# Optimization experiments

Hardware: AMD Instinct MI355X
Metric: run time of the kernel (lower is better)

Reference implementation:

```python
import jax, jax.numpy as jnp
import numpy as np

B, HK, HV, DK, DV, K = 256, 16, 32, 128, 128, 4
QKV = DK * HK * 2 + DV * HV  # 8192
EPS = 1e-6


def setup_inputs() -> dict:
    key = jax.random.key(0)
    ks = jax.random.split(key, 8)
    return dict(
        mixed_qkv=jax.random.normal(ks[0], (B, QKV), jnp.float32),
        a=jax.random.normal(ks[1], (B, HV), jnp.float32),
        b=jax.random.normal(ks[2], (B, HV), jnp.float32),
        conv_state=jax.random.normal(ks[3], (B, QKV, K - 1), jnp.float32),
        conv_weights=jax.random.normal(ks[4], (QKV, K), jnp.float32) * 0.1,
        dt_bias=jax.random.normal(ks[5], (HV,), jnp.float32),
        alog=jax.random.normal(ks[6], (HV,), jnp.float32) * 0.1,
        ssm_state=jax.random.normal(ks[7], (B, HV, DK, DV), jnp.float32) * 0.05,
    )


def reference(mixed_qkv, a, b, conv_state, conv_weights, dt_bias, alog, ssm_state):
    # --- causal_conv1d_update (decode step, seq=1): window = [cached K-1 steps, new token]
    x_cat = jnp.concatenate([conv_state, mixed_qkv[:, :, None]], axis=-1)  # [B, QKV, K]
    conv_out = jax.nn.silu(jnp.einsum('bck,ck->bc', x_cat, conv_weights))  # [B, QKV]

    # --- split q/k/v heads
    qkv = conv_out.reshape(B, 2 * HK + HV, DK)
    q, k, v = qkv[:, :HK], qkv[:, HK:2 * HK], qkv[:, 2 * HK:]  # [B,HK,DK]x2, [B,HV,DV]

    # --- fused_gdn_gating: g = -exp(A_log) * softplus(a + dt_bias); beta = sigmoid(b)
    g = -jnp.exp(alog)[None, :] * jax.nn.softplus(a + dt_bias[None, :])  # [B, HV]
    beta = jax.nn.sigmoid(b)  # [B, HV]

    # --- GQA expand k heads -> v heads
    rep = HV // HK
    q = jnp.repeat(q, rep, axis=1)  # [B, HV, DK]
    k = jnp.repeat(k, rep, axis=1)

    # --- qk l2-norm (in-kernel) + default scale d_k^-0.5 on q
    q = q / jnp.sqrt(jnp.sum(q * q, axis=-1, keepdims=True) + EPS)
    k = k / jnp.sqrt(jnp.sum(k * k, axis=-1, keepdims=True) + EPS)
    q = q * (DK ** -0.5)

    # --- single-step gated delta rule recurrence
    S = ssm_state * jnp.exp(g)[:, :, None, None]          # decay: [B,HV,DK,DV]
    kv_mem = jnp.einsum('bhkv,bhk->bhv', S, k)            # k^T S
    dv = (v - kv_mem) * beta[:, :, None]                  # delta correction
    S = S + k[:, :, :, None] * dv[:, :, None, :]          # rank-1 update
    o = jnp.einsum('bhkv,bhk->bhv', S, q)                 # [B, HV, DV]
    return o
```

## Files before the change

kernel.cpp:

```cpp
#include <hip/hip_runtime.h>
#include <math.h>

#define NB   256
#define NHK  16
#define NHV  32
#define NDK  128
#define NDV  128
#define NQKV 8192

__global__ __launch_bounds__(256) void gdn_decode_kernel(
    const float* __restrict__ mixed_qkv,
    const float* __restrict__ a_in,
    const float* __restrict__ b_in,
    const float* __restrict__ conv_state,
    const float* __restrict__ conv_w,
    const float* __restrict__ dt_bias,
    const float* __restrict__ alog,
    const float* __restrict__ ssm_state,
    float* __restrict__ out)
{
    const int bh  = blockIdx.x;
    const int b   = bh >> 5;
    const int h   = bh & 31;
    const int tid = threadIdx.x;

    __shared__ float qL[NDK], kL[NDK], vL[NDV];
    __shared__ float redq[128], redk[128], redqk[128];
    __shared__ __align__(16) float p1[8][NDV];
    __shared__ __align__(16) float p2[8][NDV];
    __shared__ float sc[2];

    for (int i = tid; i < 384; i += 256) {
        int seg  = i >> 7;
        int lane = i & 127;
        int head = (seg == 0) ? (h >> 1) : (seg == 1 ? 16 + (h >> 1) : 32 + h);
        int c    = head * 128 + lane;
        const float* cs = conv_state + ((size_t)b * NQKV + c) * 3;
        const float* w  = conv_w + (size_t)c * 4;
        float x   = mixed_qkv[(size_t)b * NQKV + c];
        float pre = cs[0]*w[0] + cs[1]*w[1] + cs[2]*w[2] + x*w[3];
        float y   = pre / (1.0f + expf(-pre));
        if (seg == 0)      qL[lane] = y;
        else if (seg == 1) kL[lane] = y;
        else               vL[lane] = y;
    }
    if (tid == 0) {
        float av = a_in[bh] + dt_bias[h];
        float sp = fmaxf(av, 0.0f) + log1pf(expf(-fabsf(av)));
        float g  = -expf(alog[h]) * sp;
        sc[0] = expf(g);
        sc[1] = 1.0f / (1.0f + expf(-b_in[bh]));
    }
    __syncthreads();

    if (tid < 128) {
        float qv   = qL[tid];
        redq[tid]  = qv * qv;
        redqk[tid] = qv * kL[tid];
    } else {
        float kv        = kL[tid - 128];
        redk[tid - 128] = kv * kv;
    }
    __syncthreads();
    for (int s = 64; s > 0; s >>= 1) {
        if (tid < s) { redq[tid] += redq[tid + s]; redqk[tid] += redqk[tid + s]; }
        else if (tid >= 128 && tid < 128 + s) { redk[tid-128] += redk[tid-128+s]; }
        __syncthreads();
    }
    const float invq = (1.0f / sqrtf(redq[0] + 1e-6f)) * 0.08838834764831845f;
    const float invk =  1.0f / sqrtf(redk[0] + 1e-6f);
    const float kq   = redqk[0] * invq * invk;
    if (tid < 128) qL[tid] *= invq;
    else           kL[tid - 128] *= invk;
    __syncthreads();

    const int vg = tid & 31;
    const int ks = tid >> 5;
    const float4* Srow = (const float4*)(ssm_state + (size_t)bh * NDK * NDV);
    float4 a1 = make_float4(0.f,0.f,0.f,0.f);
    float4 a2 = make_float4(0.f,0.f,0.f,0.f);
    #pragma unroll
    for (int kk = 0; kk < 16; ++kk) {
        int k = ks * 16 + kk;
        float4 s = Srow[k * 32 + vg];
        float kw = kL[k], qw = qL[k];
        a1.x = fmaf(s.x, kw, a1.x); a1.y = fmaf(s.y, kw, a1.y);
        a1.z = fmaf(s.z, kw, a1.z); a1.w = fmaf(s.w, kw, a1.w);
        a2.x = fmaf(s.x, qw, a2.x); a2.y = fmaf(s.y, qw, a2.y);
        a2.z = fmaf(s.z, qw, a2.z); a2.w = fmaf(s.w, qw, a2.w);
    }
    *(float4*)&p1[ks][vg * 4] = a1;
    *(float4*)&p2[ks][vg * 4] = a2;
    __syncthreads();

    if (tid < 128) {
        float t1 = 0.f, t2 = 0.f;
        #pragma unroll
        for (int s = 0; s < 8; ++s) { t1 += p1[s][tid]; t2 += p2[s][tid]; }
        const float eg   = sc[0];
        const float beta = sc[1];
        float dv = (vL[tid] - eg * t1) * beta;
        out[(size_t)bh * NDV + tid] = fmaf(eg, t2, kq * dv);
    }
}

extern "C" void kernel_launch(void* const* d_in, const int* in_sizes, int n_in,
                              void* d_out, int out_size, void* d_ws, size_t ws_size,
                              hipStream_t stream) {
    const float* mixed = (const float*)d_in[0];
    const float* a     = (const float*)d_in[1];
    const float* bg    = (const float*)d_in[2];
    const float* cs    = (const float*)d_in[3];
    const float* cw    = (const float*)d_in[4];
    const float* dtb   = (const float*)d_in[5];
    const float* al    = (const float*)d_in[6];
    const float* ssm   = (const float*)d_in[7];
    float* out = (float*)d_out;

    gdn_decode_kernel<<<NB * NHV, 256, 0, stream>>>(mixed, a, bg, cs, cw, dtb, al, ssm, out);
}
```

Baseline: 103.5 us.

## Process both GQA value heads per block sharing q/k conv and norm

```diff
diff --git a/kernel.cpp b/kernel.cpp
--- a/kernel.cpp
+++ b/kernel.cpp
@@ -7,6 +7,8 @@
 #define NDK  128
 #define NDV  128
 #define NQKV 8192
+
+typedef float f32x4 __attribute__((ext_vector_type(4)));
 
 __global__ __launch_bounds__(256) void gdn_decode_kernel(
     const float* __restrict__ mixed_qkv,
@@ -19,21 +21,25 @@
     const float* __restrict__ ssm_state,
     float* __restrict__ out)
 {
-    const int bh  = blockIdx.x;
-    const int b   = bh >> 5;
-    const int h   = bh & 31;
+    const int bid = blockIdx.x;
+    const int b   = bid >> 4;
+    const int hk  = bid & 15;
     const int tid = threadIdx.x;
+    const int h0  = 2 * hk;
+    const size_t bh0 = (size_t)b * NHV + h0;
 
-    __shared__ float qL[NDK], kL[NDK], vL[NDV];
+    __shared__ float qL[NDK], kL[NDK], vL[2][NDV];
     __shared__ float redq[128], redk[128], redqk[128];
     __shared__ __align__(16) float p1[8][NDV];
     __shared__ __align__(16) float p2[8][NDV];
-    __shared__ float sc[2];
+    __shared__ float sc_eg[2], sc_beta[2];
 
-    for (int i = tid; i < 384; i += 256) {
+    #pragma unroll
+    for (int ii = 0; ii < 2; ++ii) {
+        int i    = tid + ii * 256;
         int seg  = i >> 7;
         int lane = i & 127;
-        int head = (seg == 0) ? (h >> 1) : (seg == 1 ? 16 + (h >> 1) : 32 + h);
+        int head = (seg == 0) ? hk : (seg == 1) ? (16 + hk) : (32 + h0 + (seg - 2));
         int c    = head * 128 + lane;
         const float* cs = conv_state + ((size_t)b * NQKV + c) * 3;
         const float* w  = conv_w + (size_t)c * 4;
@@ -42,14 +48,16 @@
         float y   = pre / (1.0f + expf(-pre));
         if (seg == 0)      qL[lane] = y;
         else if (seg == 1) kL[lane] = y;
-        else               vL[lane] = y;
+        else               vL[seg - 2][lane] = y;
     }
-    if (tid == 0) {
+    if (tid < 2) {
+        size_t bh = bh0 + tid;
+        int    h  = h0 + tid;
         float av = a_in[bh] + dt_bias[h];
         float sp = fmaxf(av, 0.0f) + log1pf(expf(-fabsf(av)));
         float g  = -expf(alog[h]) * sp;
-        sc[0] = expf(g);
-        sc[1] = 1.0f / (1.0f + expf(-b_in[bh]));
+        sc_eg[tid]   = expf(g);
+        sc_beta[tid] = 1.0f / (1.0f + expf(-b_in[bh]));
     }
     __syncthreads();
 
@@ -76,31 +84,46 @@
 
     const int vg = tid & 31;
     const int ks = tid >> 5;
-    const float4* Srow = (const float4*)(ssm_state + (size_t)bh * NDK * NDV);
-    float4 a1 = make_float4(0.f,0.f,0.f,0.f);
-    float4 a2 = make_float4(0.f,0.f,0.f,0.f);
+    const f32x4* S0 = (const f32x4*)(ssm_state + bh0 * (NDK * NDV));
+    const f32x4* S1 = S0 + (NDK * NDV / 4);
+    f32x4 a1_0 = {0.f,0.f,0.f,0.f}, a2_0 = {0.f,0.f,0.f,0.f};
+    f32x4 a1_1 = {0.f,0.f,0.f,0.f}, a2_1 = {0.f,0.f,0.f,0.f};
     #pragma unroll
     for (int kk = 0; kk < 16; ++kk) {
         int k = ks * 16 + kk;
-        float4 s = Srow[k * 32 + vg];
+        f32x4 s0 = __builtin_nontemporal_load(&S0[k * 32 + vg]);
+        f32x4 s1 = __builtin_nontemporal_load(&S1[k * 32 + vg]);
         float kw = kL[k], qw = qL[k];
-        a1.x = fmaf(s.x, kw, a1.x); a1.y = fmaf(s.y, kw, a1.y);
-        a1.z = fmaf(s.z, kw, a1.z); a1.w = fmaf(s.w, kw, a1.w);
-        a2.x = fmaf(s.x, qw, a2.x); a2.y = fmaf(s.y, qw, a2.y);
-        a2.z = fmaf(s.z, qw, a2.z); a2.w = fmaf(s.w, qw, a2.w);
+        a1_0 += s0 * kw;
+        a2_0 += s0 * qw;
+        a1_1 += s1 * kw;
+        a2_1 += s1 * qw;
     }
-    *(float4*)&p1[ks][vg * 4] = a1;
-    *(float4*)&p2[ks][vg * 4] = a2;
+
+    *(f32x4*)&p1[ks][vg * 4] = a1_0;
+    *(f32x4*)&p2[ks][vg * 4] = a2_0;
     __syncthreads();
-
     if (tid < 128) {
         float t1 = 0.f, t2 = 0.f;
         #pragma unroll
         for (int s = 0; s < 8; ++s) { t1 += p1[s][tid]; t2 += p2[s][tid]; }
-        const float eg   = sc[0];
-        const float beta = sc[1];
-        float dv = (vL[tid] - eg * t1) * beta;
-        out[(size_t)bh * NDV + tid] = fmaf(eg, t2, kq * dv);
+        const float eg   = sc_eg[0];
+        const float beta = sc_beta[0];
+        float dv = (vL[0][tid] - eg * t1) * beta;
+        out[bh0 * NDV + tid] = fmaf(eg, t2, kq * dv);
+    }
+    __syncthreads();
+    *(f32x4*)&p1[ks][vg * 4] = a1_1;
+    *(f32x4*)&p2[ks][vg * 4] = a2_1;
+    __syncthreads();
+    if (tid < 128) {
+        float t1 = 0.f, t2 = 0.f;
+        #pragma unroll
+        for (int s = 0; s < 8; ++s) { t1 += p1[s][tid]; t2 += p2[s][tid]; }
+        const float eg   = sc_eg[1];
+        const float beta = sc_beta[1];
+        float dv = (vL[1][tid] - eg * t1) * beta;
+        out[(bh0 + 1) * NDV + tid] = fmaf(eg, t2, kq * dv);
     }
 }
 
@@ -117,5 +140,5 @@
     const float* ssm   = (const float*)d_in[7];
     float* out = (float*)d_out;
 
-    gdn_decode_kernel<<<NB * NHV, 256, 0, stream>>>(mixed, a, bg, cs, cw, dtb, al, ssm, out);
+    gdn_decode_kernel<<<NB * NHK, 256, 0, stream>>>(mixed, a, bg, cs, cw, dtb, al, ssm, out);
 }
```

Measured after the change: 97.75 us. 1.06x faster.
